# Kernel tuning notes

Measured on AMD Instinct MI355X. Metric: run time of the kernel, lower is better.

The kernel has to match this reference:

```python
import jax, jax.numpy as jnp
import numpy as np

B, CE, CD = 4, 128, 256
HE = WE = 256
HD = WD = 128
N = CE // 8  # 16


def _up2_align_corners(x):
    # bilinear upsample x2 with align_corners=True (matches nn.UpsamplingBilinear2d)
    def axis_up(x, axis, n_in):
        n_out = 2 * n_in
        pos = jnp.arange(n_out, dtype=x.dtype) * ((n_in - 1) / (n_out - 1))
        i0 = jnp.clip(jnp.floor(pos).astype(jnp.int32), 0, n_in - 1)
        i1 = jnp.clip(i0 + 1, 0, n_in - 1)
        w = pos - i0.astype(x.dtype)
        shape = [1] * x.ndim
        shape[axis] = n_out
        w = w.reshape(shape)
        return jnp.take(x, i0, axis=axis) * (1 - w) + jnp.take(x, i1, axis=axis) * w
    x = axis_up(x, 2, x.shape[2])
    return axis_up(x, 3, x.shape[3])


def _conv7(x, w, b):
    y = jax.lax.conv_general_dilated(x, w, (1, 1), [(3, 3), (3, 3)],
                                     dimension_numbers=('NCHW', 'OIHW', 'NCHW'))
    return y + b.reshape(1, -1, 1, 1)


def _sag_branch(x, w1, b1, w2, b2):
    mx = jnp.max(x, axis=1, keepdims=True)           # channel max-pool [B,1,H,W]
    av = jnp.mean(x, axis=1, keepdims=True)          # channel avg-pool
    c1 = jnp.einsum('bchw,oc->bohw', x, w1) + b1.reshape(1, -1, 1, 1)  # 1x1 conv -> 1 ch
    return _conv7(jnp.concatenate([mx, av, c1], axis=1), w2, b2)       # [B,1,H,W]


def _cag_branch(x, wa, ba, wm, bm):
    av = jnp.mean(x, axis=(2, 3))                    # [B,C] global avg
    mx = jnp.max(x, axis=(2, 3))                     # [B,C] global max
    return av @ wa.T + ba + mx @ wm.T + bm           # [B,N]


def setup_inputs() -> dict:
    key = jax.random.key(0)
    ks = jax.random.split(key, 20)
    s = 0.02
    return {
        'x_enc': jax.random.normal(ks[0], (B, CE, HE, WE), jnp.float32),
        'x_dec': jax.random.normal(ks[1], (B, CD, HD, WD), jnp.float32),
        'cw_ea': jax.random.normal(ks[2], (N, CE), jnp.float32) * s,
        'cb_ea': jnp.zeros((N,), jnp.float32),
        'cw_em': jax.random.normal(ks[3], (N, CE), jnp.float32) * s,
        'cb_em': jnp.zeros((N,), jnp.float32),
        'cw_da': jax.random.normal(ks[4], (N, CD), jnp.float32) * s,
        'cb_da': jnp.zeros((N,), jnp.float32),
        'cw_dm': jax.random.normal(ks[5], (N, CD), jnp.float32) * s,
        'cb_dm': jnp.zeros((N,), jnp.float32),
        'cw_f': jax.random.normal(ks[6], (CE, N), jnp.float32) * s,
        'cb_f': jnp.zeros((CE,), jnp.float32),
        'sw1_e': jax.random.normal(ks[7], (1, CE), jnp.float32) * s,
        'sb1_e': jnp.zeros((1,), jnp.float32),
        'sw2_e': jax.random.normal(ks[8], (1, 3, 7, 7), jnp.float32) * s,
        'sb2_e': jnp.zeros((1,), jnp.float32),
        'sw1_d': jax.random.normal(ks[9], (1, CD), jnp.float32) * s,
        'sb1_d': jnp.zeros((1,), jnp.float32),
        'sw2_d': jax.random.normal(ks[10], (1, 3, 7, 7), jnp.float32) * s,
        'sb2_d': jnp.zeros((1,), jnp.float32),
        'save_attention': 0,
    }


def reference(x_enc, x_dec, cw_ea, cb_ea, cw_em, cb_em, cw_da, cb_da, cw_dm, cb_dm,
              cw_f, cb_f, sw1_e, sb1_e, sw2_e, sb2_e, sw1_d, sb1_d, sw2_d, sb2_d,
              save_attention):
    # decoder path: upsample x2 (align_corners=True) + ReLU
    dec_feat = jax.nn.relu(_up2_align_corners(x_dec))  # [B,CD,2HD,2WD]
    # encoder path: center crop to match
    h2, w2 = 2 * x_dec.shape[2], 2 * x_dec.shape[3]
    s0 = (x_enc.shape[2] - h2) // 2
    s1 = (x_enc.shape[3] - w2) // 2
    enc_feat = x_enc[:, :, s0:s0 + h2, s1:s1 + w2]
    # spatial attention gate (sAG)
    spat = jax.nn.sigmoid(_sag_branch(enc_feat, sw1_e, sb1_e, sw2_e, sb2_e)
                          + _sag_branch(dec_feat, sw1_d, sb1_d, sw2_d, sb2_d))  # [B,1,H,W]
    # channel attention gate (cAG)
    ce = _cag_branch(enc_feat, cw_ea, cb_ea, cw_em, cb_em)  # [B,N]
    cd = _cag_branch(dec_feat, cw_da, cb_da, cw_dm, cb_dm)  # [B,N]
    ch = jax.nn.sigmoid((ce + cd) @ cw_f.T + cb_f)           # [B,CE]
    return enc_feat * spat * ch[:, :, None, None]
```

## Files before the change

### kernel.cpp

```cpp
#include <hip/hip_runtime.h>
#include <math.h>

static const int B_  = 4;
static const int CE_ = 128;
static const int CD_ = 256;
static const int HE_ = 256;
static const int HD_ = 128;
static const int N_  = 16;
#define PLANE  65536
#define DPLANE 16384
#define UPSCALE (127.0f/255.0f)

__device__ __forceinline__ float4 fmax4(float4 a, float4 b) {
  return make_float4(fmaxf(a.x, b.x), fmaxf(a.y, b.y), fmaxf(a.z, b.z), fmaxf(a.w, b.w));
}
__device__ __forceinline__ float4 fadd4(float4 a, float4 b) {
  return make_float4(a.x + b.x, a.y + b.y, a.z + b.z, a.w + b.w);
}

__global__ __launch_bounds__(256) void k_stats(
    const float* __restrict__ xe, const float* __restrict__ xd,
    const float* __restrict__ sw1e, const float* __restrict__ sb1e,
    const float* __restrict__ sw1d, const float* __restrict__ sb1d,
    float* __restrict__ stats, float* __restrict__ eav, float* __restrict__ emx,
    float* __restrict__ dav, float* __restrict__ dmx) {
  __shared__ float smem[4864];
  int blk = blockIdx.x;
  int t = threadIdx.x;

  if (blk < 1024) {
    int b = blk >> 8, h = blk & 255;
    float bias = sb1d[0];
    float* swt  = smem;
    float* bufA = smem + 256;
    float* bufB = smem + 1280;
    swt[t] = sw1d[t];
    float ph = (float)h * UPSCALE;
    int ih0 = (int)ph; float wh = ph - (float)ih0;
    int ih1 = min(ih0 + 1, HD_ - 1);
    int rowoff = (ih1 - ih0) * HD_;
    float pw = (float)t * UPSCALE;
    int iw0 = (int)pw; float ww = pw - (float)iw0;
    int iw1 = min(iw0 + 1, HD_ - 1);
    const float* xb = xd + (size_t)b * CD_ * DPLANE + ih0 * HD_;
    int li = min(t, DPLANE - ih0 * HD_ - 1);
    float pre0 = xb[li];
    float pre1 = xb[DPLANE + li];
    float pre2 = xb[2 * DPLANE + li];
    float pre3 = xb[3 * DPLANE + li];
    float mx = -INFINITY, sm = 0.f, pj = 0.f;
    for (int p = 0; p < 64; ++p) {
      float* bw = (p & 1) ? bufB : bufA;
      bw[t] = pre0; bw[256 + t] = pre1; bw[512 + t] = pre2; bw[768 + t] = pre3;
      if (p + 1 < 64) {
        const float* nx = xb + (size_t)(4 * (p + 1)) * DPLANE;
        pre0 = nx[li];
        pre1 = nx[DPLANE + li];
        pre2 = nx[2 * DPLANE + li];
        pre3 = nx[3 * DPLANE + li];
      }
      __syncthreads();
#pragma unroll
      for (int j = 0; j < 4; ++j) {
        const float* bb = bw + j * 256;
        float l00 = bb[iw0], l01 = bb[iw1];
        float l10 = bb[rowoff + iw0], l11 = bb[rowoff + iw1];
        float top = l00 + ww * (l01 - l00);
        float bot = l10 + ww * (l11 - l10);
        float v = fmaxf(top + wh * (bot - top), 0.f);
        mx = fmaxf(mx, v);
        sm += v;
        pj = fmaf(v, swt[4 * p + j], pj);
      }
    }
    size_t o = (((size_t)b * 6 + 3) * HE_ + h) * (size_t)HE_ + t;
    stats[o] = mx;
    stats[o + (size_t)PLANE] = sm * (1.f / CD_);
    stats[o + 2 * (size_t)PLANE] = pj + bias;

  } else if (blk < 2048) {
    int bc = blk - 1024;
    const float* plane = xd + (size_t)bc * DPLANE;
    float* stage = smem;
    float* ss = smem + 4352;
    float* sx = smem + 4608;
    float pw = (float)t * UPSCALE;
    int iw0 = (int)pw; float ww = pw - (float)iw0;
    int iw1 = min(iw0 + 1, HD_ - 1);
    float sm = 0.f, m = -INFINITY;
    for (int k = 0; k < 4; ++k) {
      int w0   = (k == 0) ? 0 : (32 * k - 1);
      int rend = (k == 3) ? 128 : (32 * (k + 1) + 1);
      int nf = (rend - w0) * HD_;
      __syncthreads();
      for (int idx = t; idx < nf; idx += 256) stage[idx] = plane[w0 * HD_ + idx];
      __syncthreads();
      int h0 = 64 * k;
#pragma unroll 4
      for (int hh = h0; hh < h0 + 64; ++hh) {
        float ph = (float)hh * UPSCALE;
        int ih0 = (int)ph; float wh = ph - (float)ih0;
        int r0 = (ih0 - w0) * HD_;
        int r1 = (min(ih0 + 1, HD_ - 1) - w0) * HD_;
        float top = stage[r0 + iw0] * (1.f - ww) + stage[r0 + iw1] * ww;
        float bot = stage[r1 + iw0] * (1.f - ww) + stage[r1 + iw1] * ww;
        float v = fmaxf((1.f - wh) * top + wh * bot, 0.f);
        sm += v;
        m = fmaxf(m, v);
      }
    }
    __syncthreads();
    ss[t] = sm; sx[t] = m;
    __syncthreads();
    for (int s = 128; s > 0; s >>= 1) {
      if (t < s) { ss[t] += ss[t + s]; sx[t] = fmaxf(sx[t], sx[t + s]); }
      __syncthreads();
    }
    if (t == 0) { dav[bc] = ss[0] * (1.f / PLANE); dmx[bc] = sx[0]; }

  } else if (blk < 2560) {
    int bc = blk - 2048;
    const float4* p = (const float4*)(xe + (size_t)bc * PLANE);
    float sm = 0.f, m = -INFINITY;
    for (int i = t; i < PLANE / 4; i += 256) {
      float4 v = p[i];
      sm += (v.x + v.y) + (v.z + v.w);
      m = fmaxf(m, fmaxf(fmaxf(v.x, v.y), fmaxf(v.z, v.w)));
    }
    float* ss = smem;
    float* sx = smem + 256;
    ss[t] = sm; sx[t] = m;
    __syncthreads();
    for (int s = 128; s > 0; s >>= 1) {
      if (t < s) { ss[t] += ss[t + s]; sx[t] = fmaxf(sx[t], sx[t + s]); }
      __syncthreads();
    }
    if (t == 0) { eav[bc] = ss[0] * (1.f / PLANE); emx[bc] = sx[0]; }

  } else {
    int bh = blk - 2560;
    int b = bh >> 8, h = bh & 255;
    int cs = t >> 6, q = t & 63;
    float bias = sb1e[0];
    float*  wt  = smem;
    float4* red = (float4*)(smem + 128);
    if (t < CE_) wt[t] = sw1e[t];
    __syncthreads();
    const float4* base = (const float4*)xe + (size_t)b * CE_ * (PLANE / 4)
                         + (size_t)h * 64 + q;
    float4 mx4 = make_float4(-INFINITY, -INFINITY, -INFINITY, -INFINITY);
    float4 sm4 = make_float4(0.f, 0.f, 0.f, 0.f);
    float4 pj4 = make_float4(0.f, 0.f, 0.f, 0.f);
#pragma unroll 4
    for (int c = cs; c < CE_; c += 4) {
      float4 v = base[(size_t)c * (PLANE / 4)];
      float wc = wt[c];
      mx4 = fmax4(mx4, v);
      sm4 = fadd4(sm4, v);
      pj4.x = fmaf(v.x, wc, pj4.x); pj4.y = fmaf(v.y, wc, pj4.y);
      pj4.z = fmaf(v.z, wc, pj4.z); pj4.w = fmaf(v.w, wc, pj4.w);
    }
    red[t] = mx4; red[256 + t] = sm4; red[512 + t] = pj4;
    __syncthreads();
    if (t < 64) {
      float4 m = fmax4(fmax4(red[t], red[t + 64]),
                       fmax4(red[t + 128], red[t + 192]));
      float4 s = fadd4(fadd4(red[256 + t], red[256 + t + 64]),
                       fadd4(red[256 + t + 128], red[256 + t + 192]));
      float4 p = fadd4(fadd4(red[512 + t], red[512 + t + 64]),
                       fadd4(red[512 + t + 128], red[512 + t + 192]));
      float4* so = (float4*)stats;
      size_t o4 = (size_t)(b * 6) * (PLANE / 4) + (size_t)h * 64 + t;
      so[o4] = m;
      s.x *= (1.f / CE_); s.y *= (1.f / CE_); s.z *= (1.f / CE_); s.w *= (1.f / CE_);
      so[o4 + PLANE / 4] = s;
      p.x += bias; p.y += bias; p.z += bias; p.w += bias;
      so[o4 + 2 * (PLANE / 4)] = p;
    }
  }
}

__global__ __launch_bounds__(256) void k_gate(
    const float* __restrict__ stats,
    const float* __restrict__ we, const float* __restrict__ be,
    const float* __restrict__ wd, const float* __restrict__ bd,
    const float* __restrict__ eav, const float* __restrict__ emx,
    const float* __restrict__ dav, const float* __restrict__ dmx,
    const float* __restrict__ cw_ea, const float* __restrict__ cb_ea,
    const float* __restrict__ cw_em, const float* __restrict__ cb_em,
    const float* __restrict__ cw_da, const float* __restrict__ cb_da,
    const float* __restrict__ cw_dm, const float* __restrict__ cb_dm,
    const float* __restrict__ cw_f, const float* __restrict__ cb_f,
    const float* __restrict__ x, float* __restrict__ out) {
  int bh = blockIdx.x;
  int b = bh >> 8, h = bh & 255;
  int t = threadIdx.x;
  int w = t;

  __shared__ float swE[147], swD[147];
  __shared__ float part[16][17];
  __shared__ float s_n[16];
  __shared__ float s_ch[128];
  __shared__ float s_spat[256];

  if (t < 147) { swE[t] = we[t]; swD[t] = wd[t]; }

  {
    int n = t & 15, sl = t >> 4;
    const float* ea = eav + b * CE_;
    const float* em = emx + b * CE_;
    const float* da = dav + b * CD_;
    const float* dm = dmx + b * CD_;
    float p = 0.f;
#pragma unroll
    for (int i = 0; i < 8; ++i) {
      int c = sl * 8 + i;
      p = fmaf(ea[c], cw_ea[n * CE_ + c], p);
      p = fmaf(em[c], cw_em[n * CE_ + c], p);
    }
#pragma unroll
    for (int i = 0; i < 16; ++i) {
      int c = sl * 16 + i;
      p = fmaf(da[c], cw_da[n * CD_ + c], p);
      p = fmaf(dm[c], cw_dm[n * CD_ + c], p);
    }
    part[n][sl] = p;
  }
  __syncthreads();
  if (t < 16) {
    float s = cb_ea[t] + cb_em[t] + cb_da[t] + cb_dm[t];
#pragma unroll
    for (int sl = 0; sl < 16; ++sl) s += part[t][sl];
    s_n[t] = s;
  }
  __syncthreads();
  if (t < 128) {
    float s = cb_f[t];
#pragma unroll
    for (int n = 0; n < N_; ++n) s = fmaf(s_n[n], cw_f[t * N_ + n], s);
    s_ch[t] = 1.f / (1.f + __expf(-s));
  }

  float acc = be[0] + bd[0];
  const float* sb = stats + ((size_t)b * 6) * PLANE;
#pragma unroll
  for (int ic = 0; ic < 3; ++ic) {
    const float* pe = sb + (size_t)ic * PLANE;
    const float* pd = sb + (size_t)(ic + 3) * PLANE;
#pragma unroll
    for (int ky = 0; ky < 7; ++ky) {
      int y = h + ky - 3;
      if ((unsigned)y >= 256u) continue;
      const float* rowE = pe + y * 256;
      const float* rowD = pd + y * 256;
#pragma unroll
      for (int kx = 0; kx < 7; ++kx) {
        int xw = w + kx - 3;
        if ((unsigned)xw >= 256u) continue;
        float we_ = swE[ic * 49 + ky * 7 + kx];
        float wd_ = swD[ic * 49 + ky * 7 + kx];
        acc = fmaf(rowE[xw], we_, acc);
        acc = fmaf(rowD[xw], wd_, acc);
      }
    }
  }
  s_spat[w] = 1.f / (1.f + __expf(-acc));
  __syncthreads();

  int w4 = t & 63;
  int cq = t >> 6;
  float4 sv = ((const float4*)s_spat)[w4];
  const float4* xp = (const float4*)x + ((size_t)b * CE_) * (PLANE / 4) + h * 64;
  float4*       op = (float4*)out     + ((size_t)b * CE_) * (PLANE / 4) + h * 64;
  for (int c = cq; c < CE_; c += 4) {
    float cv = s_ch[c];
    float4 xv = xp[(size_t)c * (PLANE / 4) + w4];
    float4 o;
    o.x = xv.x * sv.x * cv;
    o.y = xv.y * sv.y * cv;
    o.z = xv.z * sv.z * cv;
    o.w = xv.w * sv.w * cv;
    op[(size_t)c * (PLANE / 4) + w4] = o;
  }
}

extern "C" void kernel_launch(void* const* d_in, const int* in_sizes, int n_in,
                              void* d_out, int out_size, void* d_ws, size_t ws_size,
                              hipStream_t stream) {
  const float* x_enc = (const float*)d_in[0];
  const float* x_dec = (const float*)d_in[1];
  const float* cw_ea = (const float*)d_in[2];
  const float* cb_ea = (const float*)d_in[3];
  const float* cw_em = (const float*)d_in[4];
  const float* cb_em = (const float*)d_in[5];
  const float* cw_da = (const float*)d_in[6];
  const float* cb_da = (const float*)d_in[7];
  const float* cw_dm = (const float*)d_in[8];
  const float* cb_dm = (const float*)d_in[9];
  const float* cw_f  = (const float*)d_in[10];
  const float* cb_f  = (const float*)d_in[11];
  const float* sw1_e = (const float*)d_in[12];
  const float* sb1_e = (const float*)d_in[13];
  const float* sw2_e = (const float*)d_in[14];
  const float* sb2_e = (const float*)d_in[15];
  const float* sw1_d = (const float*)d_in[16];
  const float* sb1_d = (const float*)d_in[17];
  const float* sw2_d = (const float*)d_in[18];
  const float* sb2_d = (const float*)d_in[19];
  float* out = (float*)d_out;
  (void)in_sizes; (void)n_in; (void)out_size; (void)ws_size;

  float* ws    = (float*)d_ws;
  float* stats = ws;
  float* eav   = ws + 1572864;
  float* emx   = eav + 512;
  float* dav   = emx + 512;
  float* dmx   = dav + 1024;

  k_stats<<<3584, 256, 0, stream>>>(x_enc, x_dec, sw1_e, sb1_e, sw1_d, sb1_d,
                                    stats, eav, emx, dav, dmx);
  k_gate <<<B_ * HE_, 256, 0, stream>>>(stats, sw2_e, sb2_e, sw2_d, sb2_d,
                                        eav, emx, dav, dmx,
                                        cw_ea, cb_ea, cw_em, cb_em,
                                        cw_da, cb_da, cw_dm, cb_dm,
                                        cw_f, cb_f, x_enc, out);
}
```

Measured before the change: 407.3 us.

## Stage conv stats tiles in LDS, two rows per gate block, reorder stats blocks

The gate kernel now processes two output rows per 512-thread block and first stages the 8-row halo of all six stat planes into shared memory, so the 7x7 conv reads LDS instead of global memory. The stats kernel reorders its block ranges so the heavy encoder-projection blocks are scheduled first. The decoder upsample path now loads 8 channels per double-buffer step and uses precomputed bilinear weights. The cost targeted is redundant global reads in the conv and scheduling imbalance. The trade-off is 48KB of shared memory per gate block, which lowers occupancy.

```diff
diff --git a/kernel.cpp b/kernel.cpp
--- a/kernel.cpp
+++ b/kernel.cpp
@@ -30,116 +30,6 @@
 
   if (blk < 1024) {
     int b = blk >> 8, h = blk & 255;
-    float bias = sb1d[0];
-    float* swt  = smem;
-    float* bufA = smem + 256;
-    float* bufB = smem + 1280;
-    swt[t] = sw1d[t];
-    float ph = (float)h * UPSCALE;
-    int ih0 = (int)ph; float wh = ph - (float)ih0;
-    int ih1 = min(ih0 + 1, HD_ - 1);
-    int rowoff = (ih1 - ih0) * HD_;
-    float pw = (float)t * UPSCALE;
-    int iw0 = (int)pw; float ww = pw - (float)iw0;
-    int iw1 = min(iw0 + 1, HD_ - 1);
-    const float* xb = xd + (size_t)b * CD_ * DPLANE + ih0 * HD_;
-    int li = min(t, DPLANE - ih0 * HD_ - 1);
-    float pre0 = xb[li];
-    float pre1 = xb[DPLANE + li];
-    float pre2 = xb[2 * DPLANE + li];
-    float pre3 = xb[3 * DPLANE + li];
-    float mx = -INFINITY, sm = 0.f, pj = 0.f;
-    for (int p = 0; p < 64; ++p) {
-      float* bw = (p & 1) ? bufB : bufA;
-      bw[t] = pre0; bw[256 + t] = pre1; bw[512 + t] = pre2; bw[768 + t] = pre3;
-      if (p + 1 < 64) {
-        const float* nx = xb + (size_t)(4 * (p + 1)) * DPLANE;
-        pre0 = nx[li];
-        pre1 = nx[DPLANE + li];
-        pre2 = nx[2 * DPLANE + li];
-        pre3 = nx[3 * DPLANE + li];
-      }
-      __syncthreads();
-#pragma unroll
-      for (int j = 0; j < 4; ++j) {
-        const float* bb = bw + j * 256;
-        float l00 = bb[iw0], l01 = bb[iw1];
-        float l10 = bb[rowoff + iw0], l11 = bb[rowoff + iw1];
-        float top = l00 + ww * (l01 - l00);
-        float bot = l10 + ww * (l11 - l10);
-        float v = fmaxf(top + wh * (bot - top), 0.f);
-        mx = fmaxf(mx, v);
-        sm += v;
-        pj = fmaf(v, swt[4 * p + j], pj);
-      }
-    }
-    size_t o = (((size_t)b * 6 + 3) * HE_ + h) * (size_t)HE_ + t;
-    stats[o] = mx;
-    stats[o + (size_t)PLANE] = sm * (1.f / CD_);
-    stats[o + 2 * (size_t)PLANE] = pj + bias;
-
-  } else if (blk < 2048) {
-    int bc = blk - 1024;
-    const float* plane = xd + (size_t)bc * DPLANE;
-    float* stage = smem;
-    float* ss = smem + 4352;
-    float* sx = smem + 4608;
-    float pw = (float)t * UPSCALE;
-    int iw0 = (int)pw; float ww = pw - (float)iw0;
-    int iw1 = min(iw0 + 1, HD_ - 1);
-    float sm = 0.f, m = -INFINITY;
-    for (int k = 0; k < 4; ++k) {
-      int w0   = (k == 0) ? 0 : (32 * k - 1);
-      int rend = (k == 3) ? 128 : (32 * (k + 1) + 1);
-      int nf = (rend - w0) * HD_;
-      __syncthreads();
-      for (int idx = t; idx < nf; idx += 256) stage[idx] = plane[w0 * HD_ + idx];
-      __syncthreads();
-      int h0 = 64 * k;
-#pragma unroll 4
-      for (int hh = h0; hh < h0 + 64; ++hh) {
-        float ph = (float)hh * UPSCALE;
-        int ih0 = (int)ph; float wh = ph - (float)ih0;
-        int r0 = (ih0 - w0) * HD_;
-        int r1 = (min(ih0 + 1, HD_ - 1) - w0) * HD_;
-        float top = stage[r0 + iw0] * (1.f - ww) + stage[r0 + iw1] * ww;
-        float bot = stage[r1 + iw0] * (1.f - ww) + stage[r1 + iw1] * ww;
-        float v = fmaxf((1.f - wh) * top + wh * bot, 0.f);
-        sm += v;
-        m = fmaxf(m, v);
-      }
-    }
-    __syncthreads();
-    ss[t] = sm; sx[t] = m;
-    __syncthreads();
-    for (int s = 128; s > 0; s >>= 1) {
-      if (t < s) { ss[t] += ss[t + s]; sx[t] = fmaxf(sx[t], sx[t + s]); }
-      __syncthreads();
-    }
-    if (t == 0) { dav[bc] = ss[0] * (1.f / PLANE); dmx[bc] = sx[0]; }
-
-  } else if (blk < 2560) {
-    int bc = blk - 2048;
-    const float4* p = (const float4*)(xe + (size_t)bc * PLANE);
-    float sm = 0.f, m = -INFINITY;
-    for (int i = t; i < PLANE / 4; i += 256) {
-      float4 v = p[i];
-      sm += (v.x + v.y) + (v.z + v.w);
-      m = fmaxf(m, fmaxf(fmaxf(v.x, v.y), fmaxf(v.z, v.w)));
-    }
-    float* ss = smem;
-    float* sx = smem + 256;
-    ss[t] = sm; sx[t] = m;
-    __syncthreads();
-    for (int s = 128; s > 0; s >>= 1) {
-      if (t < s) { ss[t] += ss[t + s]; sx[t] = fmaxf(sx[t], sx[t + s]); }
-      __syncthreads();
-    }
-    if (t == 0) { eav[bc] = ss[0] * (1.f / PLANE); emx[bc] = sx[0]; }
-
-  } else {
-    int bh = blk - 2560;
-    int b = bh >> 8, h = bh & 255;
     int cs = t >> 6, q = t & 63;
     float bias = sb1e[0];
     float*  wt  = smem;
@@ -177,10 +67,132 @@
       p.x += bias; p.y += bias; p.z += bias; p.w += bias;
       so[o4 + 2 * (PLANE / 4)] = p;
     }
-  }
-}
-
-__global__ __launch_bounds__(256) void k_gate(
+
+  } else if (blk < 2048) {
+    int bh = blk - 1024;
+    int b = bh >> 8, h = bh & 255;
+    float bias = sb1d[0];
+    float* swt  = smem;
+    float* bufA = smem + 256;
+    float* bufB = smem + 2304;
+    swt[t] = sw1d[t];
+    float ph = (float)h * UPSCALE;
+    int ih0 = (int)ph; float wh = ph - (float)ih0;
+    int ih1 = min(ih0 + 1, HD_ - 1);
+    int rowoff = (ih1 - ih0) * HD_;
+    float pw = (float)t * UPSCALE;
+    int iw0 = (int)pw; float ww = pw - (float)iw0;
+    int iw1 = min(iw0 + 1, HD_ - 1);
+    float w00 = (1.f - wh) * (1.f - ww), w01 = (1.f - wh) * ww;
+    float w10 = wh * (1.f - ww),        w11 = wh * ww;
+    const float* xb = xd + (size_t)b * CD_ * DPLANE + ih0 * HD_;
+    int li = min(t, DPLANE - ih0 * HD_ - 1);
+    float p0 = xb[li];
+    float p1 = xb[DPLANE + li];
+    float p2 = xb[2 * DPLANE + li];
+    float p3 = xb[3 * DPLANE + li];
+    float p4 = xb[4 * DPLANE + li];
+    float p5 = xb[5 * DPLANE + li];
+    float p6 = xb[6 * DPLANE + li];
+    float p7 = xb[7 * DPLANE + li];
+    float mx = -INFINITY, sm = 0.f, pj = 0.f;
+    for (int p = 0; p < 32; ++p) {
+      float* bw = (p & 1) ? bufB : bufA;
+      bw[t] = p0;          bw[256 + t] = p1;
+      bw[512 + t] = p2;    bw[768 + t] = p3;
+      bw[1024 + t] = p4;   bw[1280 + t] = p5;
+      bw[1536 + t] = p6;   bw[1792 + t] = p7;
+      if (p + 1 < 32) {
+        const float* nx = xb + (size_t)(8 * (p + 1)) * DPLANE;
+        p0 = nx[li];
+        p1 = nx[DPLANE + li];
+        p2 = nx[2 * DPLANE + li];
+        p3 = nx[3 * DPLANE + li];
+        p4 = nx[4 * DPLANE + li];
+        p5 = nx[5 * DPLANE + li];
+        p6 = nx[6 * DPLANE + li];
+        p7 = nx[7 * DPLANE + li];
+      }
+      __syncthreads();
+#pragma unroll
+      for (int j = 0; j < 8; ++j) {
+        const float* bb = bw + j * 256;
+        float l00 = bb[iw0], l01 = bb[iw1];
+        float l10 = bb[rowoff + iw0], l11 = bb[rowoff + iw1];
+        float v = w00 * l00 + w01 * l01 + w10 * l10 + w11 * l11;
+        v = fmaxf(v, 0.f);
+        mx = fmaxf(mx, v);
+        sm += v;
+        pj = fmaf(v, swt[8 * p + j], pj);
+      }
+    }
+    size_t o = (((size_t)b * 6 + 3) * HE_ + h) * (size_t)HE_ + t;
+    stats[o] = mx;
+    stats[o + (size_t)PLANE] = sm * (1.f / CD_);
+    stats[o + 2 * (size_t)PLANE] = pj + bias;
+
+  } else if (blk < 3072) {
+    int bc = blk - 2048;
+    const float* plane = xd + (size_t)bc * DPLANE;
+    float* stage = smem;
+    float* ss = smem + 4352;
+    float* sx = smem + 4608;
+    float pw = (float)t * UPSCALE;
+    int iw0 = (int)pw; float ww = pw - (float)iw0;
+    int iw1 = min(iw0 + 1, HD_ - 1);
+    float sm = 0.f, m = -INFINITY;
+    for (int k = 0; k < 4; ++k) {
+      int w0   = (k == 0) ? 0 : (32 * k - 1);
+      int rend = (k == 3) ? 128 : (32 * (k + 1) + 1);
+      int nf = (rend - w0) * HD_;
+      __syncthreads();
+      for (int idx = t; idx < nf; idx += 256) stage[idx] = plane[w0 * HD_ + idx];
+      __syncthreads();
+      int h0 = 64 * k;
+#pragma unroll 4
+      for (int hh = h0; hh < h0 + 64; ++hh) {
+        float ph = (float)hh * UPSCALE;
+        int ih0 = (int)ph; float wh = ph - (float)ih0;
+        int r0 = (ih0 - w0) * HD_;
+        int r1 = (min(ih0 + 1, HD_ - 1) - w0) * HD_;
+        float top = stage[r0 + iw0] * (1.f - ww) + stage[r0 + iw1] * ww;
+        float bot = stage[r1 + iw0] * (1.f - ww) + stage[r1 + iw1] * ww;
+        float v = fmaxf((1.f - wh) * top + wh * bot, 0.f);
+        sm += v;
+        m = fmaxf(m, v);
+      }
+    }
+    __syncthreads();
+    ss[t] = sm; sx[t] = m;
+    __syncthreads();
+    for (int s = 128; s > 0; s >>= 1) {
+      if (t < s) { ss[t] += ss[t + s]; sx[t] = fmaxf(sx[t], sx[t + s]); }
+      __syncthreads();
+    }
+    if (t == 0) { dav[bc] = ss[0] * (1.f / PLANE); dmx[bc] = sx[0]; }
+
+  } else {
+    int bc = blk - 3072;
+    const float4* p = (const float4*)(xe + (size_t)bc * PLANE);
+    float sm = 0.f, m = -INFINITY;
+    for (int i = t; i < PLANE / 4; i += 256) {
+      float4 v = p[i];
+      sm += (v.x + v.y) + (v.z + v.w);
+      m = fmaxf(m, fmaxf(fmaxf(v.x, v.y), fmaxf(v.z, v.w)));
+    }
+    float* ss = smem;
+    float* sx = smem + 256;
+    ss[t] = sm; sx[t] = m;
+    __syncthreads();
+    for (int s = 128; s > 0; s >>= 1) {
+      if (t < s) { ss[t] += ss[t + s]; sx[t] = fmaxf(sx[t], sx[t + s]); }
+      __syncthreads();
+    }
+    if (t == 0) { eav[bc] = ss[0] * (1.f / PLANE); emx[bc] = sx[0]; }
+  }
+}
+
+__global__ __launch_bounds__(512) void k_gate(
     const float* __restrict__ stats,
     const float* __restrict__ we, const float* __restrict__ be,
     const float* __restrict__ wd, const float* __restrict__ bd,
@@ -192,20 +204,31 @@
     const float* __restrict__ cw_dm, const float* __restrict__ cb_dm,
     const float* __restrict__ cw_f, const float* __restrict__ cb_f,
     const float* __restrict__ x, float* __restrict__ out) {
-  int bh = blockIdx.x;
-  int b = bh >> 8, h = bh & 255;
+  int blk = blockIdx.x;
+  int b = blk >> 7, h0 = (blk & 127) * 2;
   int t = threadIdx.x;
-  int w = t;
-
+  int rho = t >> 8, tw = t & 255;
+
+  __shared__ float st[12288];
   __shared__ float swE[147], swD[147];
   __shared__ float part[16][17];
   __shared__ float s_n[16];
   __shared__ float s_ch[128];
-  __shared__ float s_spat[256];
+  __shared__ float s_spat[512];
 
   if (t < 147) { swE[t] = we[t]; swD[t] = wd[t]; }
 
   {
+    const float* sbase = stats + (size_t)b * 6 * PLANE;
+    for (int idx = t; idx < 12288; idx += 512) {
+      int ic = idx >> 11, j = (idx >> 8) & 7, w = idx & 255;
+      int y = h0 - 3 + j;
+      st[idx] = ((unsigned)y < 256u)
+                  ? sbase[((size_t)ic << 16) + (size_t)y * 256 + w] : 0.f;
+    }
+  }
+
+  if (t < 256) {
     int n = t & 15, sl = t >> 4;
     const float* ea = eav + b * CE_;
     const float* em = emx + b * CE_;
@@ -242,36 +265,30 @@
   }
 
   float acc = be[0] + bd[0];
-  const float* sb = stats + ((size_t)b * 6) * PLANE;
 #pragma unroll
   for (int ic = 0; ic < 3; ++ic) {
-    const float* pe = sb + (size_t)ic * PLANE;
-    const float* pd = sb + (size_t)(ic + 3) * PLANE;
 #pragma unroll
     for (int ky = 0; ky < 7; ++ky) {
-      int y = h + ky - 3;
-      if ((unsigned)y >= 256u) continue;
-      const float* rowE = pe + y * 256;
-      const float* rowD = pd + y * 256;
+      const float* rE = st + (ic * 8 + rho + ky) * 256;
+      const float* rD = st + ((ic + 3) * 8 + rho + ky) * 256;
 #pragma unroll
       for (int kx = 0; kx < 7; ++kx) {
-        int xw = w + kx - 3;
+        int xw = tw + kx - 3;
         if ((unsigned)xw >= 256u) continue;
-        float we_ = swE[ic * 49 + ky * 7 + kx];
-        float wd_ = swD[ic * 49 + ky * 7 + kx];
-        acc = fmaf(rowE[xw], we_, acc);
-        acc = fmaf(rowD[xw], wd_, acc);
+        acc = fmaf(rE[xw], swE[ic * 49 + ky * 7 + kx], acc);
+        acc = fmaf(rD[xw], swD[ic * 49 + ky * 7 + kx], acc);
       }
     }
   }
-  s_spat[w] = 1.f / (1.f + __expf(-acc));
+  s_spat[rho * 256 + tw] = 1.f / (1.f + __expf(-acc));
   __syncthreads();
 
   int w4 = t & 63;
-  int cq = t >> 6;
-  float4 sv = ((const float4*)s_spat)[w4];
-  const float4* xp = (const float4*)x + ((size_t)b * CE_) * (PLANE / 4) + h * 64;
-  float4*       op = (float4*)out     + ((size_t)b * CE_) * (PLANE / 4) + h * 64;
+  int cq = (t >> 6) & 3;
+  int hr = h0 + rho;
+  float4 sv = ((const float4*)s_spat)[rho * 64 + w4];
+  const float4* xp = (const float4*)x + ((size_t)b * CE_) * (PLANE / 4) + hr * 64;
+  float4*       op = (float4*)out     + ((size_t)b * CE_) * (PLANE / 4) + hr * 64;
   for (int c = cq; c < CE_; c += 4) {
     float cv = s_ch[c];
     float4 xv = xp[(size_t)c * (PLANE / 4) + w4];
@@ -319,7 +336,7 @@
 
   k_stats<<<3584, 256, 0, stream>>>(x_enc, x_dec, sw1_e, sb1_e, sw1_d, sb1_d,
                                     stats, eav, emx, dav, dmx);
-  k_gate <<<B_ * HE_, 256, 0, stream>>>(stats, sw2_e, sb2_e, sw2_d, sb2_d,
+  k_gate <<<B_ * 128, 512, 0, stream>>>(stats, sw2_e, sb2_e, sw2_d, sb2_d,
                                         eav, emx, dav, dmx,
                                         cw_ea, cb_ea, cw_em, cb_em,
                                         cw_da, cb_da, cw_dm, cb_dm,
```

Result: no change. 414.6 us (+1.8%).
